# Kernel optimization log

Hardware: AMD Instinct MI355X
Metric: run time of the kernel (lower is better)

## Reference

```python
import jax, jax.numpy as jnp
import numpy as np

N_NODES = 100000
N_EDGES = 1000000
D_IN, D_HID, D_OUT = 20, 64, 64
NEG_SLOPE = 0.2


def _gat_layer(x, src, dst, W, a_src, a_dst, b, n_nodes):
    """PyG-style single-head GATConv: message j->i, softmax over incoming edges of i."""
    h = x @ W                                  # [N, D]
    alpha_s = h @ a_src                        # [N]
    alpha_d = h @ a_dst                        # [N]
    e = jax.nn.leaky_relu(alpha_s[src] + alpha_d[dst], NEG_SLOPE)  # [E]
    # numerically-stable segment softmax over destination nodes
    m = jax.ops.segment_max(e, dst, num_segments=n_nodes)          # [N]
    ex = jnp.exp(e - m[dst])                                       # [E]
    denom = jax.ops.segment_sum(ex, dst, num_segments=n_nodes)     # [N]
    alpha = ex / denom[dst]                                        # [E]
    out = jax.ops.segment_sum(alpha[:, None] * h[src], dst, num_segments=n_nodes)
    return out + b


def setup_inputs() -> dict:
    key = jax.random.key(0)
    ks = jax.random.split(key, 11)
    x = jax.random.normal(ks[0], (N_NODES, D_IN), dtype=jnp.float32)
    edge_index = jax.random.randint(ks[1], (2, N_EDGES), 0, N_NODES, dtype=jnp.int64)
    s1 = 1.0 / np.sqrt(D_IN)
    s2 = 1.0 / np.sqrt(D_HID)
    return {
        "x": x,
        "edge_index": edge_index,
        "W1": jax.random.normal(ks[2], (D_IN, D_HID), dtype=jnp.float32) * s1,
        "a_src1": jax.random.normal(ks[3], (D_HID,), dtype=jnp.float32) * s2,
        "a_dst1": jax.random.normal(ks[4], (D_HID,), dtype=jnp.float32) * s2,
        "b1": jnp.zeros((D_HID,), dtype=jnp.float32),
        "W2": jax.random.normal(ks[5], (D_HID, D_OUT), dtype=jnp.float32) * s2,
        "a_src2": jax.random.normal(ks[6], (D_OUT,), dtype=jnp.float32) * s2,
        "a_dst2": jax.random.normal(ks[7], (D_OUT,), dtype=jnp.float32) * s2,
        "b2": jnp.zeros((D_OUT,), dtype=jnp.float32),
    }


def reference(x, edge_index, W1, a_src1, a_dst1, b1, W2, a_src2, a_dst2, b2):
    n = x.shape[0]
    # PyG GATConv adds self-loops by default
    loops = jnp.arange(n, dtype=edge_index.dtype)
    src = jnp.concatenate([edge_index[0], loops])
    dst = jnp.concatenate([edge_index[1], loops])
    h = _gat_layer(x, src, dst, W1, a_src1, a_dst1, b1, n)
    h = jax.nn.relu(h)
    # dropout(p=0.2) is identity in eval mode
    h = _gat_layer(h, src, dst, W2, a_src2, a_dst2, b2, n)
    # global_mean_pool with all-zero batch -> mean over all nodes, shape [1, D_OUT]
    return jnp.mean(h, axis=0, keepdims=True)
```

## Files before the change

kernel.cpp:

```cpp
#include <hip/hip_runtime.h>
#include <math.h>

#define NDIM 64
#define LRELU_SLOPE 0.2f
#define BSHIFT 8
#define BNODES 256
#define ECAP 3584
#define CCAP (ECAP + BNODES)

typedef float f32x2 __attribute__((ext_vector_type(2)));

__device__ __forceinline__ ushort f2bf(float f) {
    unsigned u = __float_as_uint(f);
    unsigned r = (u + 0x7fffu + ((u >> 16) & 1u)) >> 16;
    return (ushort)r;
}
__device__ __forceinline__ float bflo(unsigned u) { return __uint_as_float(u << 16); }
__device__ __forceinline__ float bfhi(unsigned u) { return __uint_as_float(u & 0xffff0000u); }

__global__ void initb_kernel(int* __restrict__ bcur, int nb) {
    int i = blockIdx.x * blockDim.x + threadIdx.x;
    if (i < nb) bcur[i] = i * ECAP;
}

__global__ __launch_bounds__(256) void pg_kernel(
    const int* __restrict__ src, const int* __restrict__ dst,
    int* __restrict__ bcur, unsigned* __restrict__ part, int E, int nb, int PB,
    const float* __restrict__ X, const float* __restrict__ W,
    const float* __restrict__ asrc, const float* __restrict__ adst,
    unsigned char* __restrict__ h, float* __restrict__ as_,
    float* __restrict__ ad_, int N) {
    int t = threadIdx.x;
    if ((int)blockIdx.x < PB) {
        __shared__ int hist[512];
        __shared__ int base[512];
        for (int i = t; i < nb; i += 256) hist[i] = 0;
        __syncthreads();
        int chunk = blockIdx.x * 4096;
        int s[16], d[16];
#pragma unroll
        for (int j = 0; j < 4; ++j) {
            int idx = chunk + j * 1024 + t * 4;
            if (idx + 3 < E) {
                int4 sv = *(const int4*)(src + idx);
                int4 dv = *(const int4*)(dst + idx);
                s[j*4+0]=sv.x; s[j*4+1]=sv.y; s[j*4+2]=sv.z; s[j*4+3]=sv.w;
                d[j*4+0]=dv.x; d[j*4+1]=dv.y; d[j*4+2]=dv.z; d[j*4+3]=dv.w;
            } else {
#pragma unroll
                for (int q = 0; q < 4; ++q) {
                    int i2 = idx + q;
                    if (i2 < E) { s[j*4+q] = src[i2]; d[j*4+q] = dst[i2]; }
                    else        { s[j*4+q] = 0;       d[j*4+q] = -1; }
                }
            }
        }
#pragma unroll
        for (int j = 0; j < 16; ++j)
            if (d[j] >= 0) atomicAdd(&hist[d[j] >> BSHIFT], 1);
        __syncthreads();
        for (int i = t; i < nb; i += 256) {
            int c = hist[i];
            base[i] = c ? atomicAdd(&bcur[i], c) : 0;
            hist[i] = 0;
        }
        __syncthreads();
#pragma unroll
        for (int j = 0; j < 16; ++j) {
            if (d[j] >= 0) {
                int b = d[j] >> BSHIFT;
                int pos = base[b] + atomicAdd(&hist[b], 1);
                int lim = (b + 1) * ECAP - 1;
                if (pos > lim) pos = lim;
                part[pos] = ((unsigned)(d[j] & (BNODES - 1)) << 17) | (unsigned)s[j];
            }
        }
    } else {
        const int K = 20, KS = 32;
        __shared__ float xs[64 * 32];
        __shared__ unsigned hsq[64 * 17];
        __shared__ float ps[2][4][64];
        int base2 = (blockIdx.x - PB) * 64;
        for (int i = t; i < 64 * KS; i += 256) {
            int nl = i / KS, k = i - nl * KS;
            int node = base2 + nl;
            float v = (k < K && node < N) ? X[(size_t)node * K + k] : 0.f;
            xs[nl * KS + ((k + nl) & (KS - 1))] = v;
        }
        __syncthreads();
        int wid = __builtin_amdgcn_readfirstlane(t >> 6);
        int lane = t & 63;
        int node = base2 + lane;
        float acc[16];
#pragma unroll
        for (int j = 0; j < 16; ++j) acc[j] = 0.f;
        const float* Wg = W + wid * 16;
        const float* xrow = xs + lane * KS;
#pragma unroll 4
        for (int k = 0; k < K; ++k) {
            float xk = xrow[(k + lane) & (KS - 1)];
#pragma unroll
            for (int j = 0; j < 16; ++j)
                acc[j] = fmaf(xk, Wg[k * 64 + j], acc[j]);
        }
        float s = 0.f, d = 0.f;
#pragma unroll
        for (int j = 0; j < 16; ++j) {
            s = fmaf(acc[j], asrc[wid * 16 + j], s);
            d = fmaf(acc[j], adst[wid * 16 + j], d);
        }
        ps[0][wid][lane] = s;
        ps[1][wid][lane] = d;
#pragma unroll
        for (int j = 0; j < 16; j += 4) {
            int q = (wid * 16 + j) >> 2;
            int sp = (q + lane) & 15;
            int u = __builtin_amdgcn_cvt_pk_fp8_f32(acc[j], acc[j + 1], 0, false);
            u = __builtin_amdgcn_cvt_pk_fp8_f32(acc[j + 2], acc[j + 3], u, true);
            hsq[lane * 17 + sp] = (unsigned)u;
        }
        __syncthreads();
        if (wid == 0) {
            float s4 = ps[0][0][lane] + ps[0][1][lane] + ps[0][2][lane] + ps[0][3][lane];
            float d4 = ps[1][0][lane] + ps[1][1][lane] + ps[1][2][lane] + ps[1][3][lane];
            if (node < N) { as_[node] = s4; ad_[node] = d4; }
        }
        unsigned* hout = (unsigned*)h;
        for (int pass = 0; pass < 4; ++pass) {
            int row = pass * 16 + (t >> 4);
            int q = t & 15;
            int sp = (q + row) & 15;
            unsigned v = hsq[row * 17 + sp];
            int n2 = base2 + row;
            if (n2 < N) hout[(size_t)n2 * 16 + q] = v;
        }
    }
}

__global__ __launch_bounds__(256) void csr_kernel(
    const int* __restrict__ bcur, const unsigned* __restrict__ part,
    int* __restrict__ csr, int2* __restrict__ offlen, int N) {
    __shared__ int hist[256];
    __shared__ int sc[256];
    int b = blockIdx.x, t = threadIdx.x;
    int nodeBase = b << BSHIFT;
    int nNodes = min(BNODES, N - nodeBase);
    int count = min(bcur[b] - b * ECAP, ECAP);
    hist[t] = (t < nNodes) ? 1 : 0;
    __syncthreads();
    const unsigned* slice = part + (size_t)b * ECAP;
    for (int i = t; i < count; i += 256) {
        int dl = (int)(slice[i] >> 17);
        atomicAdd(&hist[dl], 1);
    }
    __syncthreads();
    int cnt = hist[t];
    sc[t] = cnt;
    __syncthreads();
    for (int o = 1; o < 256; o <<= 1) {
        int v = sc[t];
        int u = (t >= o) ? sc[t - o] : 0;
        __syncthreads();
        sc[t] = v + u;
        __syncthreads();
    }
    int excl = sc[t] - cnt;
    int boff = b * CCAP;
    if (t < nNodes) {
        offlen[nodeBase + t] = make_int2(boff + excl, cnt);
        csr[boff + excl] = nodeBase + t;
    }
    hist[t] = excl + 1;
    __syncthreads();
    for (int i = t; i < count; i += 256) {
        unsigned e = slice[i];
        int dl = (int)(e >> 17);
        int pos = boff + atomicAdd(&hist[dl], 1);
        csr[pos] = (int)(e & 0x1ffffu);
    }
}

template<int K, int KS, bool BF16IN>
__global__ __launch_bounds__(256) void gemm_kernel(
    const void* __restrict__ Xv, const float* __restrict__ W,
    const float* __restrict__ asrc, const float* __restrict__ adst,
    unsigned char* __restrict__ h, float* __restrict__ as_, float* __restrict__ ad_, int N) {
    __shared__ float xs[64 * KS];
    __shared__ unsigned hsq[64 * 17];
    __shared__ float ps[2][4][64];
    int t = threadIdx.x;
    int base = blockIdx.x * 64;
    if (BF16IN) {
        const unsigned* X = (const unsigned*)Xv;
        for (int i = t; i < 64 * (K / 2); i += 256) {
            int nl = i / (K / 2), p = i - nl * (K / 2);
            int k = p * 2;
            int node = base + nl;
            unsigned u = (node < N) ? X[(size_t)node * (K / 2) + p] : 0u;
            xs[nl * KS + ((k + nl) & (KS - 1))] = bflo(u);
            xs[nl * KS + ((k + 1 + nl) & (KS - 1))] = bfhi(u);
        }
    } else {
        const float* X = (const float*)Xv;
        for (int i = t; i < 64 * KS; i += 256) {
            int nl = i / KS, k = i - nl * KS;
            int node = base + nl;
            float v = (k < K && node < N) ? X[(size_t)node * K + k] : 0.f;
            xs[nl * KS + ((k + nl) & (KS - 1))] = v;
        }
    }
    __syncthreads();
    int wid = __builtin_amdgcn_readfirstlane(t >> 6);
    int lane = t & 63;
    int node = base + lane;
    float acc[16];
#pragma unroll
    for (int j = 0; j < 16; ++j) acc[j] = 0.f;
    const float* Wg = W + wid * 16;
    const float* xrow = xs + lane * KS;
#pragma unroll 4
    for (int k = 0; k < K; ++k) {
        float xk = xrow[(k + lane) & (KS - 1)];
#pragma unroll
        for (int j = 0; j < 16; ++j)
            acc[j] = fmaf(xk, Wg[k * 64 + j], acc[j]);
    }
    float s = 0.f, d = 0.f;
#pragma unroll
    for (int j = 0; j < 16; ++j) {
        s = fmaf(acc[j], asrc[wid * 16 + j], s);
        d = fmaf(acc[j], adst[wid * 16 + j], d);
    }
    ps[0][wid][lane] = s;
    ps[1][wid][lane] = d;
#pragma unroll
    for (int j = 0; j < 16; j += 4) {
        int q = (wid * 16 + j) >> 2;
        int sp = (q + lane) & 15;
        int u = __builtin_amdgcn_cvt_pk_fp8_f32(acc[j], acc[j + 1], 0, false);
        u = __builtin_amdgcn_cvt_pk_fp8_f32(acc[j + 2], acc[j + 3], u, true);
        hsq[lane * 17 + sp] = (unsigned)u;
    }
    __syncthreads();
    if (wid == 0) {
        float s4 = ps[0][0][lane] + ps[0][1][lane] + ps[0][2][lane] + ps[0][3][lane];
        float d4 = ps[1][0][lane] + ps[1][1][lane] + ps[1][2][lane] + ps[1][3][lane];
        if (node < N) { as_[node] = s4; ad_[node] = d4; }
    }
    unsigned* hout = (unsigned*)h;
    for (int pass = 0; pass < 4; ++pass) {
        int row = pass * 16 + (t >> 4);
        int q = t & 15;
        int sp = (q + row) & 15;
        unsigned v = hsq[row * 17 + sp];
        int n2 = base + row;
        if (n2 < N) hout[(size_t)n2 * 16 + q] = v;
    }
}

__global__ __launch_bounds__(256) void agg_kernel(
    const int2* __restrict__ offlen, const int* __restrict__ csr,
    const float* __restrict__ as_, const float* __restrict__ ad_,
    const unsigned char* __restrict__ hsrc, const float* __restrict__ bias,
    ushort* __restrict__ out, float* __restrict__ pool, int n, int mode) {
    __shared__ float psum[8][NDIM];
    int wid = threadIdx.x >> 6, lane = threadIdx.x & 63;
    int half = lane >> 5;
    int g = (lane >> 3) & 3;
    int l = lane & 7;
    int node = blockIdx.x * 8 + wid * 2 + half;
    float v[8];
#pragma unroll
    for (int j = 0; j < 8; ++j) v[j] = 0.f;
    if (node < n) {
        int2 ol = offlen[node];
        int off = ol.x, len = ol.y;
        float adi = ad_[node];
        float acc[8];
#pragma unroll
        for (int j = 0; j < 8; ++j) acc[j] = 0.f;
        float den = 0.f;
        int niter = (len + 3) >> 2;
        int e0 = g, e1 = 4 + g;
        bool ve0 = e0 < len, ve1 = e1 < len;
        int sk0 = ve0 ? csr[off + e0] : 0;
        int sk1 = ve1 ? csr[off + e1] : 0;
        float a0 = ve0 ? as_[sk0] : -INFINITY;
        uint2 hv0 = make_uint2(0, 0);
        if (ve0) hv0 = *(const uint2*)(hsrc + ((size_t)sk0 << 6) + (l << 3));
        for (int i = 0; i < niter - 1; ++i) {
            int e2 = (i + 2) * 4 + g;
            bool ve2 = e2 < len;
            int sk2 = ve2 ? csr[off + e2] : 0;
            float a1 = ve1 ? as_[sk1] : -INFINITY;
            uint2 hv1 = make_uint2(0, 0);
            if (ve1) hv1 = *(const uint2*)(hsrc + ((size_t)sk1 << 6) + (l << 3));
            float tt = a0 + adi;
            tt = (tt > 0.f) ? tt : LRELU_SLOPE * tt;
            float ex = __expf(tt);
            den += ex;
            f32x2 p0 = __builtin_amdgcn_cvt_pk_f32_fp8(hv0.x, false);
            f32x2 p1 = __builtin_amdgcn_cvt_pk_f32_fp8(hv0.x, true);
            f32x2 p2 = __builtin_amdgcn_cvt_pk_f32_fp8(hv0.y, false);
            f32x2 p3 = __builtin_amdgcn_cvt_pk_f32_fp8(hv0.y, true);
            acc[0] = fmaf(ex, p0.x, acc[0]);
            acc[1] = fmaf(ex, p0.y, acc[1]);
            acc[2] = fmaf(ex, p1.x, acc[2]);
            acc[3] = fmaf(ex, p1.y, acc[3]);
            acc[4] = fmaf(ex, p2.x, acc[4]);
            acc[5] = fmaf(ex, p2.y, acc[5]);
            acc[6] = fmaf(ex, p3.x, acc[6]);
            acc[7] = fmaf(ex, p3.y, acc[7]);
            a0 = a1; hv0 = hv1;
            sk1 = sk2; ve1 = ve2;
        }
        {
            float tt = a0 + adi;
            tt = (tt > 0.f) ? tt : LRELU_SLOPE * tt;
            float ex = __expf(tt);
            den += ex;
            f32x2 p0 = __builtin_amdgcn_cvt_pk_f32_fp8(hv0.x, false);
            f32x2 p1 = __builtin_amdgcn_cvt_pk_f32_fp8(hv0.x, true);
            f32x2 p2 = __builtin_amdgcn_cvt_pk_f32_fp8(hv0.y, false);
            f32x2 p3 = __builtin_amdgcn_cvt_pk_f32_fp8(hv0.y, true);
            acc[0] = fmaf(ex, p0.x, acc[0]);
            acc[1] = fmaf(ex, p0.y, acc[1]);
            acc[2] = fmaf(ex, p1.x, acc[2]);
            acc[3] = fmaf(ex, p1.y, acc[3]);
            acc[4] = fmaf(ex, p2.x, acc[4]);
            acc[5] = fmaf(ex, p2.y, acc[5]);
            acc[6] = fmaf(ex, p3.x, acc[6]);
            acc[7] = fmaf(ex, p3.y, acc[7]);
        }
#pragma unroll
        for (int j = 0; j < 8; ++j) {
            acc[j] += __shfl_xor(acc[j], 8);
            acc[j] += __shfl_xor(acc[j], 16);
        }
        den += __shfl_xor(den, 8);
        den += __shfl_xor(den, 16);
        float inv = 1.f / den;
        const float4 bv0 = *(const float4*)(bias + l * 8);
        const float4 bv1 = *(const float4*)(bias + l * 8 + 4);
        v[0] = fmaf(acc[0], inv, bv0.x);
        v[1] = fmaf(acc[1], inv, bv0.y);
        v[2] = fmaf(acc[2], inv, bv0.z);
        v[3] = fmaf(acc[3], inv, bv0.w);
        v[4] = fmaf(acc[4], inv, bv1.x);
        v[5] = fmaf(acc[5], inv, bv1.y);
        v[6] = fmaf(acc[6], inv, bv1.z);
        v[7] = fmaf(acc[7], inv, bv1.w);
        if (mode == 1) {
#pragma unroll
            for (int j = 0; j < 8; ++j) v[j] = fmaxf(v[j], 0.f);
            if (g == 0) {
                uint4 pk;
                pk.x = (unsigned)f2bf(v[0]) | ((unsigned)f2bf(v[1]) << 16);
                pk.y = (unsigned)f2bf(v[2]) | ((unsigned)f2bf(v[3]) << 16);
                pk.z = (unsigned)f2bf(v[4]) | ((unsigned)f2bf(v[5]) << 16);
                pk.w = (unsigned)f2bf(v[6]) | ((unsigned)f2bf(v[7]) << 16);
                *(uint4*)(out + (size_t)node * NDIM + l * 8) = pk;
            }
        }
    }
    if (mode == 2) {
        int hw = wid * 2 + half;
        if (g == 0) {
#pragma unroll
            for (int j = 0; j < 8; ++j) psum[hw][l * 8 + j] = v[j];
        }
        __syncthreads();
        if (threadIdx.x < NDIM) {
            float t = 0.f;
#pragma unroll
            for (int r = 0; r < 8; ++r) t += psum[r][threadIdx.x];
            pool[(size_t)blockIdx.x * NDIM + threadIdx.x] = t;
        }
    }
}

__global__ void mean_kernel(const float* __restrict__ pool, float* __restrict__ out,
                            int nb, float invn) {
    __shared__ float sm[4][NDIM];
    int lane = threadIdx.x & 63, wid = threadIdx.x >> 6;
    int row = blockIdx.x * 4 + wid;
    int stride = gridDim.x * 4;
    float s = 0.f;
    for (int i = row; i < nb; i += stride) s += pool[(long)i * NDIM + lane];
    sm[wid][lane] = s;
    __syncthreads();
    if (wid == 0) {
        float v = sm[0][lane] + sm[1][lane] + sm[2][lane] + sm[3][lane];
        atomicAdd(&out[lane], v * invn);
    }
}

extern "C" void kernel_launch(void* const* d_in, const int* in_sizes, int n_in,
                              void* d_out, int out_size, void* d_ws, size_t ws_size,
                              hipStream_t stream) {
    const float* x      = (const float*)d_in[0];
    const int*   eidx   = (const int*)d_in[1];
    const float* W1     = (const float*)d_in[2];
    const float* a_src1 = (const float*)d_in[3];
    const float* a_dst1 = (const float*)d_in[4];
    const float* b1     = (const float*)d_in[5];
    const float* W2     = (const float*)d_in[6];
    const float* a_src2 = (const float*)d_in[7];
    const float* a_dst2 = (const float*)d_in[8];
    const float* b2     = (const float*)d_in[9];
    float* out = (float*)d_out;

    const int N = in_sizes[0] / 20;
    const int E = in_sizes[1] / 2;
    const int* src = eidx;
    const int* dst = eidx + E;
    const int NB = (N + BNODES - 1) >> BSHIFT;

    const int gemm_blocks = (N + 63) / 64;
    const int agg_blocks  = (N + 7) / 8;
    const int PB = (E + 4095) / 4096;

    char* ws = (char*)d_ws;
    unsigned char* h = (unsigned char*)ws;
    ushort* o   = (ushort*)(h + (size_t)N * NDIM);
    float* as_  = (float*)(o + (size_t)N * NDIM);
    float* ad_  = as_ + N;
    int2*  offlen = (int2*)(ad_ + N);
    int*   csr  = (int*)(offlen + N);
    float* pool = (float*)(csr + (size_t)NB * CCAP);
    int*   bcur = (int*)(pool + (size_t)agg_blocks * NDIM);
    unsigned* part = (unsigned*)(bcur + NB);

    hipMemsetAsync(d_out, 0, (size_t)out_size * sizeof(float), stream);

    initb_kernel<<<(NB + 255) / 256, 256, 0, stream>>>(bcur, NB);
    pg_kernel<<<PB + gemm_blocks, 256, 0, stream>>>(
        src, dst, bcur, part, E, NB, PB,
        x, W1, a_src1, a_dst1, h, as_, ad_, N);
    csr_kernel<<<NB, 256, 0, stream>>>(bcur, part, csr, offlen, N);

    agg_kernel<<<agg_blocks, 256, 0, stream>>>(offlen, csr, as_, ad_, h, b1, o, pool, N, 1);

    gemm_kernel<64, 64, true><<<gemm_blocks, 256, 0, stream>>>(o, W2, a_src2, a_dst2, h, as_, ad_, N);
    agg_kernel<<<agg_blocks, 256, 0, stream>>>(offlen, csr, as_, ad_, h, b2, o, pool, N, 2);

    mean_kernel<<<64, 256, 0, stream>>>(pool, out, agg_blocks, 1.0f / (float)N);
}
```

Measured before the change: 198.9 us.

## Fuse layer-2 GEMM and attention projections into layer-1 aggregation kernel

Layer-1 aggregation now applies ReLU, stages each node's 64-wide output in shared memory, and immediately multiplies by W2 (loaded into LDS per block). It computes the layer-2 src/dst attention scalars and writes FP8 h2 directly, so the separate GEMM kernel and its bf16 intermediate go away. Separate buffers for layer-1 and layer-2 features and scores avoid in-place hazards. The cost is a 16KB W2 load into LDS per 8-node block, plus extra LDS and a block-wide sync, which may reduce occupancy of the latency-bound gather kernel.

Result: slower. 212.1 us (+6.6%).

```diff
diff --git a/kernel.cpp b/kernel.cpp
--- a/kernel.cpp
+++ b/kernel.cpp
@@ -180,98 +180,29 @@
     }
 }
 
-template<int K, int KS, bool BF16IN>
-__global__ __launch_bounds__(256) void gemm_kernel(
-    const void* __restrict__ Xv, const float* __restrict__ W,
-    const float* __restrict__ asrc, const float* __restrict__ adst,
-    unsigned char* __restrict__ h, float* __restrict__ as_, float* __restrict__ ad_, int N) {
-    __shared__ float xs[64 * KS];
-    __shared__ unsigned hsq[64 * 17];
-    __shared__ float ps[2][4][64];
-    int t = threadIdx.x;
-    int base = blockIdx.x * 64;
-    if (BF16IN) {
-        const unsigned* X = (const unsigned*)Xv;
-        for (int i = t; i < 64 * (K / 2); i += 256) {
-            int nl = i / (K / 2), p = i - nl * (K / 2);
-            int k = p * 2;
-            int node = base + nl;
-            unsigned u = (node < N) ? X[(size_t)node * (K / 2) + p] : 0u;
-            xs[nl * KS + ((k + nl) & (KS - 1))] = bflo(u);
-            xs[nl * KS + ((k + 1 + nl) & (KS - 1))] = bfhi(u);
-        }
-    } else {
-        const float* X = (const float*)Xv;
-        for (int i = t; i < 64 * KS; i += 256) {
-            int nl = i / KS, k = i - nl * KS;
-            int node = base + nl;
-            float v = (k < K && node < N) ? X[(size_t)node * K + k] : 0.f;
-            xs[nl * KS + ((k + nl) & (KS - 1))] = v;
-        }
-    }
-    __syncthreads();
-    int wid = __builtin_amdgcn_readfirstlane(t >> 6);
-    int lane = t & 63;
-    int node = base + lane;
-    float acc[16];
-#pragma unroll
-    for (int j = 0; j < 16; ++j) acc[j] = 0.f;
-    const float* Wg = W + wid * 16;
-    const float* xrow = xs + lane * KS;
-#pragma unroll 4
-    for (int k = 0; k < K; ++k) {
-        float xk = xrow[(k + lane) & (KS - 1)];
-#pragma unroll
-        for (int j = 0; j < 16; ++j)
-            acc[j] = fmaf(xk, Wg[k * 64 + j], acc[j]);
-    }
-    float s = 0.f, d = 0.f;
-#pragma unroll
-    for (int j = 0; j < 16; ++j) {
-        s = fmaf(acc[j], asrc[wid * 16 + j], s);
-        d = fmaf(acc[j], adst[wid * 16 + j], d);
-    }
-    ps[0][wid][lane] = s;
-    ps[1][wid][lane] = d;
-#pragma unroll
-    for (int j = 0; j < 16; j += 4) {
-        int q = (wid * 16 + j) >> 2;
-        int sp = (q + lane) & 15;
-        int u = __builtin_amdgcn_cvt_pk_fp8_f32(acc[j], acc[j + 1], 0, false);
-        u = __builtin_amdgcn_cvt_pk_fp8_f32(acc[j + 2], acc[j + 3], u, true);
-        hsq[lane * 17 + sp] = (unsigned)u;
-    }
-    __syncthreads();
-    if (wid == 0) {
-        float s4 = ps[0][0][lane] + ps[0][1][lane] + ps[0][2][lane] + ps[0][3][lane];
-        float d4 = ps[1][0][lane] + ps[1][1][lane] + ps[1][2][lane] + ps[1][3][lane];
-        if (node < N) { as_[node] = s4; ad_[node] = d4; }
-    }
-    unsigned* hout = (unsigned*)h;
-    for (int pass = 0; pass < 4; ++pass) {
-        int row = pass * 16 + (t >> 4);
-        int q = t & 15;
-        int sp = (q + row) & 15;
-        unsigned v = hsq[row * 17 + sp];
-        int n2 = base + row;
-        if (n2 < N) hout[(size_t)n2 * 16 + q] = v;
-    }
-}
-
-__global__ __launch_bounds__(256) void agg_kernel(
+__global__ __launch_bounds__(256) void agg1g2_kernel(
     const int2* __restrict__ offlen, const int* __restrict__ csr,
     const float* __restrict__ as_, const float* __restrict__ ad_,
     const unsigned char* __restrict__ hsrc, const float* __restrict__ bias,
-    ushort* __restrict__ out, float* __restrict__ pool, int n, int mode) {
-    __shared__ float psum[8][NDIM];
-    int wid = threadIdx.x >> 6, lane = threadIdx.x & 63;
+    const float* __restrict__ W2, const float* __restrict__ asrc2,
+    const float* __restrict__ adst2,
+    unsigned char* __restrict__ h2, float* __restrict__ as2_,
+    float* __restrict__ ad2_, int n) {
+    __shared__ float W2s[64 * 64];
+    __shared__ float ot[8][68];
+    int t = threadIdx.x;
+    {
+        const float4* Wv = (const float4*)W2;
+        float4* Ws = (float4*)W2s;
+        for (int i = t; i < 64 * 16; i += 256) Ws[i] = Wv[i];
+    }
+    int wid = t >> 6, lane = t & 63;
     int half = lane >> 5;
     int g = (lane >> 3) & 3;
     int l = lane & 7;
-    int node = blockIdx.x * 8 + wid * 2 + half;
-    float v[8];
-#pragma unroll
-    for (int j = 0; j < 8; ++j) v[j] = 0.f;
+    int hw = wid * 2 + half;
+    int node = blockIdx.x * 8 + hw;
+    __syncthreads();
     if (node < n) {
         int2 ol = offlen[node];
         int off = ol.x, len = ol.y;
@@ -342,6 +273,136 @@
         float inv = 1.f / den;
         const float4 bv0 = *(const float4*)(bias + l * 8);
         const float4 bv1 = *(const float4*)(bias + l * 8 + 4);
+        float v0 = fmaxf(fmaf(acc[0], inv, bv0.x), 0.f);
+        float v1 = fmaxf(fmaf(acc[1], inv, bv0.y), 0.f);
+        float v2 = fmaxf(fmaf(acc[2], inv, bv0.z), 0.f);
+        float v3 = fmaxf(fmaf(acc[3], inv, bv0.w), 0.f);
+        float v4 = fmaxf(fmaf(acc[4], inv, bv1.x), 0.f);
+        float v5 = fmaxf(fmaf(acc[5], inv, bv1.y), 0.f);
+        float v6 = fmaxf(fmaf(acc[6], inv, bv1.z), 0.f);
+        float v7 = fmaxf(fmaf(acc[7], inv, bv1.w), 0.f);
+        if (g == 0) {
+            *(float4*)&ot[hw][l * 8]     = make_float4(v0, v1, v2, v3);
+            *(float4*)&ot[hw][l * 8 + 4] = make_float4(v4, v5, v6, v7);
+        }
+    }
+    __syncthreads();
+    if (node < n) {
+        int lh = lane & 31;
+        float acc0 = 0.f, acc1 = 0.f;
+        const float* wrow = W2s + 2 * lh;
+        const float* orow = ot[hw];
+#pragma unroll 8
+        for (int k = 0; k < 64; ++k) {
+            float ok = orow[k];
+            float2 w = *(const float2*)(wrow + (size_t)k * 64);
+            acc0 = fmaf(ok, w.x, acc0);
+            acc1 = fmaf(ok, w.y, acc1);
+        }
+        float2 av = *(const float2*)(asrc2 + 2 * lh);
+        float2 dv = *(const float2*)(adst2 + 2 * lh);
+        float sp = acc0 * av.x + acc1 * av.y;
+        float dp = acc0 * dv.x + acc1 * dv.y;
+#pragma unroll
+        for (int o = 1; o < 32; o <<= 1) {
+            sp += __shfl_xor(sp, o);
+            dp += __shfl_xor(dp, o);
+        }
+        if (lh == 0) { as2_[node] = sp; ad2_[node] = dp; }
+        float n0 = __shfl_xor(acc0, 1);
+        float n1 = __shfl_xor(acc1, 1);
+        if ((lh & 1) == 0) {
+            int u = __builtin_amdgcn_cvt_pk_fp8_f32(acc0, acc1, 0, false);
+            u = __builtin_amdgcn_cvt_pk_fp8_f32(n0, n1, u, true);
+            ((unsigned*)h2)[(size_t)node * 16 + (lh >> 1)] = (unsigned)u;
+        }
+    }
+}
+
+__global__ __launch_bounds__(256) void agg_kernel(
+    const int2* __restrict__ offlen, const int* __restrict__ csr,
+    const float* __restrict__ as_, const float* __restrict__ ad_,
+    const unsigned char* __restrict__ hsrc, const float* __restrict__ bias,
+    float* __restrict__ pool, int n) {
+    __shared__ float psum[8][NDIM];
+    int wid = threadIdx.x >> 6, lane = threadIdx.x & 63;
+    int half = lane >> 5;
+    int g = (lane >> 3) & 3;
+    int l = lane & 7;
+    int node = blockIdx.x * 8 + wid * 2 + half;
+    float v[8];
+#pragma unroll
+    for (int j = 0; j < 8; ++j) v[j] = 0.f;
+    if (node < n) {
+        int2 ol = offlen[node];
+        int off = ol.x, len = ol.y;
+        float adi = ad_[node];
+        float acc[8];
+#pragma unroll
+        for (int j = 0; j < 8; ++j) acc[j] = 0.f;
+        float den = 0.f;
+        int niter = (len + 3) >> 2;
+        int e0 = g, e1 = 4 + g;
+        bool ve0 = e0 < len, ve1 = e1 < len;
+        int sk0 = ve0 ? csr[off + e0] : 0;
+        int sk1 = ve1 ? csr[off + e1] : 0;
+        float a0 = ve0 ? as_[sk0] : -INFINITY;
+        uint2 hv0 = make_uint2(0, 0);
+        if (ve0) hv0 = *(const uint2*)(hsrc + ((size_t)sk0 << 6) + (l << 3));
+        for (int i = 0; i < niter - 1; ++i) {
+            int e2 = (i + 2) * 4 + g;
+            bool ve2 = e2 < len;
+            int sk2 = ve2 ? csr[off + e2] : 0;
+            float a1 = ve1 ? as_[sk1] : -INFINITY;
+            uint2 hv1 = make_uint2(0, 0);
+            if (ve1) hv1 = *(const uint2*)(hsrc + ((size_t)sk1 << 6) + (l << 3));
+            float tt = a0 + adi;
+            tt = (tt > 0.f) ? tt : LRELU_SLOPE * tt;
+            float ex = __expf(tt);
+            den += ex;
+            f32x2 p0 = __builtin_amdgcn_cvt_pk_f32_fp8(hv0.x, false);
+            f32x2 p1 = __builtin_amdgcn_cvt_pk_f32_fp8(hv0.x, true);
+            f32x2 p2 = __builtin_amdgcn_cvt_pk_f32_fp8(hv0.y, false);
+            f32x2 p3 = __builtin_amdgcn_cvt_pk_f32_fp8(hv0.y, true);
+            acc[0] = fmaf(ex, p0.x, acc[0]);
+            acc[1] = fmaf(ex, p0.y, acc[1]);
+            acc[2] = fmaf(ex, p1.x, acc[2]);
+            acc[3] = fmaf(ex, p1.y, acc[3]);
+            acc[4] = fmaf(ex, p2.x, acc[4]);
+            acc[5] = fmaf(ex, p2.y, acc[5]);
+            acc[6] = fmaf(ex, p3.x, acc[6]);
+            acc[7] = fmaf(ex, p3.y, acc[7]);
+            a0 = a1; hv0 = hv1;
+            sk1 = sk2; ve1 = ve2;
+        }
+        {
+            float tt = a0 + adi;
+            tt = (tt > 0.f) ? tt : LRELU_SLOPE * tt;
+            float ex = __expf(tt);
+            den += ex;
+            f32x2 p0 = __builtin_amdgcn_cvt_pk_f32_fp8(hv0.x, false);
+            f32x2 p1 = __builtin_amdgcn_cvt_pk_f32_fp8(hv0.x, true);
+            f32x2 p2 = __builtin_amdgcn_cvt_pk_f32_fp8(hv0.y, false);
+            f32x2 p3 = __builtin_amdgcn_cvt_pk_f32_fp8(hv0.y, true);
+            acc[0] = fmaf(ex, p0.x, acc[0]);
+            acc[1] = fmaf(ex, p0.y, acc[1]);
+            acc[2] = fmaf(ex, p1.x, acc[2]);
+            acc[3] = fmaf(ex, p1.y, acc[3]);
+            acc[4] = fmaf(ex, p2.x, acc[4]);
+            acc[5] = fmaf(ex, p2.y, acc[5]);
+            acc[6] = fmaf(ex, p3.x, acc[6]);
+            acc[7] = fmaf(ex, p3.y, acc[7]);
+        }
+#pragma unroll
+        for (int j = 0; j < 8; ++j) {
+            acc[j] += __shfl_xor(acc[j], 8);
+            acc[j] += __shfl_xor(acc[j], 16);
+        }
+        den += __shfl_xor(den, 8);
+        den += __shfl_xor(den, 16);
+        float inv = 1.f / den;
+        const float4 bv0 = *(const float4*)(bias + l * 8);
+        const float4 bv1 = *(const float4*)(bias + l * 8 + 4);
         v[0] = fmaf(acc[0], inv, bv0.x);
         v[1] = fmaf(acc[1], inv, bv0.y);
         v[2] = fmaf(acc[2], inv, bv0.z);
@@ -350,32 +411,18 @@
         v[5] = fmaf(acc[5], inv, bv1.y);
         v[6] = fmaf(acc[6], inv, bv1.z);
         v[7] = fmaf(acc[7], inv, bv1.w);
-        if (mode == 1) {
-#pragma unroll
-            for (int j = 0; j < 8; ++j) v[j] = fmaxf(v[j], 0.f);
-            if (g == 0) {
-                uint4 pk;
-                pk.x = (unsigned)f2bf(v[0]) | ((unsigned)f2bf(v[1]) << 16);
-                pk.y = (unsigned)f2bf(v[2]) | ((unsigned)f2bf(v[3]) << 16);
-                pk.z = (unsigned)f2bf(v[4]) | ((unsigned)f2bf(v[5]) << 16);
-                pk.w = (unsigned)f2bf(v[6]) | ((unsigned)f2bf(v[7]) << 16);
-                *(uint4*)(out + (size_t)node * NDIM + l * 8) = pk;
-            }
-        }
-    }
-    if (mode == 2) {
-        int hw = wid * 2 + half;
-        if (g == 0) {
-#pragma unroll
-            for (int j = 0; j < 8; ++j) psum[hw][l * 8 + j] = v[j];
-        }
-        __syncthreads();
-        if (threadIdx.x < NDIM) {
-            float t = 0.f;
-#pragma unroll
-            for (int r = 0; r < 8; ++r) t += psum[r][threadIdx.x];
-            pool[(size_t)blockIdx.x * NDIM + threadIdx.x] = t;
-        }
+    }
+    int hw = wid * 2 + half;
+    if (g == 0) {
+#pragma unroll
+        for (int j = 0; j < 8; ++j) psum[hw][l * 8 + j] = v[j];
+    }
+    __syncthreads();
+    if (threadIdx.x < NDIM) {
+        float t = 0.f;
+#pragma unroll
+        for (int r = 0; r < 8; ++r) t += psum[r][threadIdx.x];
+        pool[(size_t)blockIdx.x * NDIM + threadIdx.x] = t;
     }
 }
 
@@ -421,11 +468,13 @@
     const int PB = (E + 4095) / 4096;
 
     char* ws = (char*)d_ws;
-    unsigned char* h = (unsigned char*)ws;
-    ushort* o   = (ushort*)(h + (size_t)N * NDIM);
-    float* as_  = (float*)(o + (size_t)N * NDIM);
-    float* ad_  = as_ + N;
-    int2*  offlen = (int2*)(ad_ + N);
+    unsigned char* h1 = (unsigned char*)ws;
+    unsigned char* h2 = h1 + (size_t)N * NDIM;
+    float* as1  = (float*)(h2 + (size_t)N * NDIM);
+    float* ad1  = as1 + N;
+    float* as2  = ad1 + N;
+    float* ad2  = as2 + N;
+    int2*  offlen = (int2*)(ad2 + N);
     int*   csr  = (int*)(offlen + N);
     float* pool = (float*)(csr + (size_t)NB * CCAP);
     int*   bcur = (int*)(pool + (size_t)agg_blocks * NDIM);
@@ -436,13 +485,14 @@
     initb_kernel<<<(NB + 255) / 256, 256, 0, stream>>>(bcur, NB);
     pg_kernel<<<PB + gemm_blocks, 256, 0, stream>>>(
         src, dst, bcur, part, E, NB, PB,
-        x, W1, a_src1, a_dst1, h, as_, ad_, N);
+        x, W1, a_src1, a_dst1, h1, as1, ad1, N);
     csr_kernel<<<NB, 256, 0, stream>>>(bcur, part, csr, offlen, N);
 
-    agg_kernel<<<agg_blocks, 256, 0, stream>>>(offlen, csr, as_, ad_, h, b1, o, pool, N, 1);
-
-    gemm_kernel<64, 64, true><<<gemm_blocks, 256, 0, stream>>>(o, W2, a_src2, a_dst2, h, as_, ad_, N);
-    agg_kernel<<<agg_blocks, 256, 0, stream>>>(offlen, csr, as_, ad_, h, b2, o, pool, N, 2);
+    agg1g2_kernel<<<agg_blocks, 256, 0, stream>>>(
+        offlen, csr, as1, ad1, h1, b1,
+        W2, a_src2, a_dst2, h2, as2, ad2, N);
+
+    agg_kernel<<<agg_blocks, 256, 0, stream>>>(offlen, csr, as2, ad2, h2, b2, pool, N);
 
     mean_kernel<<<64, 256, 0, stream>>>(pool, out, agg_blocks, 1.0f / (float)N);
 }
```
